# Kernel optimization log

Hardware: AMD Instinct MI355X
Metric: run time of the kernel (lower is better)

Reference implementation:

```python
import jax, jax.numpy as jnp
import numpy as np

B, H, W, C1, C2 = 4, 256, 256, 256, 128
K = 128   # cells per patch (fixed for jit; original uses torch.unique)
E = 256   # emb_dim
NC = 16   # n_classes
G = 512   # n_genes
R = 64    # n_ref
HEADS = 8


def _w(k, shape):
    return jax.random.normal(k, shape, jnp.float32) / np.float32(np.sqrt(shape[-2]))


def setup_inputs() -> dict:
    key = jax.random.key(0)
    ks = jax.random.split(key, 20)
    return {
        "hd1": jax.random.normal(ks[0], (B, C1, H, W), jnp.float32),
        "h1": jax.random.normal(ks[1], (B, C2, H, W), jnp.float32),
        "ref_orig": jax.random.uniform(ks[2], (R, G), jnp.float32),
        "embed_w": _w(ks[3], (2 * (C1 + C2), E)),
        "comp_w1": _w(ks[4], (E, E)), "comp_w2": _w(ks[5], (E, NC)),
        "hist_w1": _w(ks[6], (E, E)), "hist_w2": _w(ks[7], (E, NC)),
        "genes_w1": _w(ks[8], (G, E)), "genes_w2": _w(ks[9], (E, NC)),
        "wref_w1": _w(ks[10], (3, E, E)), "wref_w2": _w(ks[11], (3, E, R)),
        "ca_wq": _w(ks[12], (3, NC, E)), "ca_wk": _w(ks[13], (3, G, E)),
        "ca_wv": _w(ks[14], (3, G, E)), "ca_wo": _w(ks[15], (3, E, G)),
        "nuclei_mask": jax.random.randint(ks[16], (B, H, W), 0, K + 1, jnp.int32),
        "n_cells": K,
    }


def _forward(hd1, h1, ref_orig, embed_w, comp_w1, comp_w2, hist_w1, hist_w2,
             genes_w1, genes_w2, wref_w1, wref_w2, ca_wq, ca_wk, ca_wv, ca_wo,
             nuclei_mask, n_cells):
    b, c1, hgt, wid = hd1.shape
    k_cells = n_cells
    # replaces the per-cell mask-multiply-sum loop with one segment reduce
    feat = jnp.concatenate([hd1, h1], axis=1)            # [B, C1+C2, H, W]
    cf = feat.shape[1]
    feat_flat = feat.transpose(0, 2, 3, 1).reshape(b * hgt * wid, cf)
    ids = nuclei_mask.reshape(b, hgt * wid)
    seg = jnp.where(ids > 0, jnp.arange(b)[:, None] * k_cells + ids - 1,
                    b * k_cells).reshape(-1)
    nseg = b * k_cells + 1                               # last bucket = background
    sums = jax.ops.segment_sum(feat_flat, seg, num_segments=nseg)[: b * k_cells]
    area = jax.ops.segment_sum(jnp.ones((seg.shape[0],), feat.dtype), seg,
                               num_segments=nseg)[: b * k_cells]
    cell_feat = sums / jnp.maximum(area, 1.0)[:, None]   # [N, Cf]
    glob = feat.mean((2, 3))                             # [B, Cf] = fv_hd1 ++ fv_h1
    all_fv = jnp.concatenate([cell_feat, jnp.repeat(glob, k_cells, axis=0)], axis=1)
    emb = all_fv @ embed_w                               # [N, E]
    emb_patches = emb.reshape(b, k_cells, -1).mean(1)    # per-patch mean embedding
    comp = jax.nn.softmax(jax.nn.relu(emb_patches @ comp_w1) @ comp_w2, axis=-1)
    comp_tiled = jnp.repeat(comp, k_cells, axis=0)       # [N, NC]
    out_cell_type = jax.nn.relu(emb @ hist_w1) @ hist_w2

    def branch(w1, w2, wq, wk, wv, wo):
        rw = jax.nn.softmax(jax.nn.relu(emb @ w1) @ w2, axis=-1)   # [N, R]
        ref_weighted = rw @ ref_orig                               # [N, G]
        dh = wq.shape[1] // HEADS
        q = (comp_tiled @ wq).reshape(-1, HEADS, dh)
        k = (ref_weighted @ wk).reshape(-1, HEADS, dh)
        v = (ref_weighted @ wv).reshape(-1, HEADS, dh)
        attn = jax.nn.softmax(jnp.einsum("qhd,khd->hqk", q, k) / float(np.sqrt(dh)), axis=-1)
        o = jnp.einsum("hqk,khd->qhd", attn, v).reshape(-1, HEADS * dh)
        return jax.nn.relu(ref_weighted + o @ wo)

    out_exprs = jax.vmap(branch)(wref_w1, wref_w2, ca_wq, ca_wk, ca_wv, ca_wo)  # [3,N,G]
    genes_h = jax.nn.relu(out_exprs[0] @ genes_w1)
    out_cell_type_expr = genes_h @ genes_w2
    return out_cell_type, out_exprs, out_cell_type_expr, genes_h, comp, area


def reference(hd1, h1, ref_orig, embed_w, comp_w1, comp_w2, hist_w1, hist_w2,
              genes_w1, genes_w2, wref_w1, wref_w2, ca_wq, ca_wk, ca_wv, ca_wo,
              nuclei_mask, n_cells):
    out_cell_type, out_exprs, out_cell_type_expr, genes_h, comp, area = _forward(
        hd1, h1, ref_orig, embed_w, comp_w1, comp_w2, hist_w1, hist_w2,
        genes_w1, genes_w2, wref_w1, wref_w2, ca_wq, ca_wk, ca_wv, ca_wo,
        nuclei_mask, n_cells)
    return (out_cell_type, out_exprs[0], out_exprs[1], out_exprs[2],
            out_cell_type_expr, genes_h, comp, area)
```

## Files before the change

kernel.cpp:

```cpp
#include <hip/hip_runtime.h>
#include <hip/hip_bf16.h>

#define Bn 4
#define C1n 256
#define C2n 128
#define CF 384
#define HWn 65536
#define Kc 128
#define Nn 512
#define En 256
#define NCn 16
#define Gn 512
#define Rn 64
#define HEADSn 8
#define DHn 32

#define CHK 32
#define PCH2 (HWn/CHK)
#define TC2 32

#define SCALE_F 1048576.0f
#define INV_SCALE (1.0f/1048576.0f)

typedef unsigned long long ull;

__global__ __launch_bounds__(256) void area_k(const int* __restrict__ mask,
                                              int* __restrict__ apart) {
    int chunk = blockIdx.x, b = blockIdx.y;
    __shared__ int hist[4][129];
    int t = threadIdx.x, w = t >> 6;
    for (int i = t; i < 4 * 129; i += 256) ((int*)hist)[i] = 0;
    __syncthreads();
    const int* mp = mask + (size_t)b * HWn + chunk * PCH2;
    #pragma unroll
    for (int it = 0; it < PCH2 / 1024; ++it) {
        int4 v = *(const int4*)(mp + it * 1024 + t * 4);
        atomicAdd(&hist[w][v.x], 1);
        atomicAdd(&hist[w][v.y], 1);
        atomicAdd(&hist[w][v.z], 1);
        atomicAdd(&hist[w][v.w], 1);
    }
    __syncthreads();
    if (t < 128)
        apart[(chunk * Bn + b) * Kc + t] =
            hist[0][t+1] + hist[1][t+1] + hist[2][t+1] + hist[3][t+1];
}

__global__ __launch_bounds__(256) void segreduce3_k(
        const float* __restrict__ hd1, const float* __restrict__ h1,
        const int* __restrict__ mask,
        int* __restrict__ spart) {
    int chunk = blockIdx.x, cg = blockIdx.y, b = blockIdx.z;
    int c0 = cg * TC2;
    const float* base = (c0 < C1n)
        ? hd1 + ((size_t)(b * C1n + c0)) * HWn
        : h1  + ((size_t)(b * C2n + (c0 - C1n))) * HWn;
    const int* mp = mask + (size_t)b * HWn + chunk * PCH2;

    __shared__ int bins[129 * 33];

    int t = threadIdx.x;
    int cL = t >> 3, l8 = t & 7;
    for (int i = t; i < 129 * 33; i += 256) bins[i] = 0;
    __syncthreads();

    const float* rowp = base + (size_t)cL * HWn;
    for (int px0 = l8 * 4; px0 < PCH2; px0 += 64) {
        float4 v0 = *(const float4*)(rowp + px0);
        float4 v1 = *(const float4*)(rowp + px0 + 32);
        int4 i0 = *(const int4*)(mp + px0);
        int4 i1 = *(const int4*)(mp + px0 + 32);
        atomicAdd(&bins[i0.x * 33 + cL], __float2int_rn(v0.x * SCALE_F));
        atomicAdd(&bins[i0.y * 33 + cL], __float2int_rn(v0.y * SCALE_F));
        atomicAdd(&bins[i0.z * 33 + cL], __float2int_rn(v0.z * SCALE_F));
        atomicAdd(&bins[i0.w * 33 + cL], __float2int_rn(v0.w * SCALE_F));
        atomicAdd(&bins[i1.x * 33 + cL], __float2int_rn(v1.x * SCALE_F));
        atomicAdd(&bins[i1.y * 33 + cL], __float2int_rn(v1.y * SCALE_F));
        atomicAdd(&bins[i1.z * 33 + cL], __float2int_rn(v1.z * SCALE_F));
        atomicAdd(&bins[i1.w * 33 + cL], __float2int_rn(v1.w * SCALE_F));
    }
    __syncthreads();
    for (int i = t; i < 129 * TC2; i += 256) {
        int cell = i >> 5, cc = i & 31;
        spart[((size_t)(chunk * Bn + b) * 129 + cell) * CF + c0 + cc] = bins[cell * 33 + cc];
    }
}

__global__ void reduce_k(const int* __restrict__ spart, float* __restrict__ ctot) {
    int idx = blockIdx.x * 256 + threadIdx.x;
    if (idx >= Bn * 129 * CF) return;
    int b = idx / (129 * CF);
    int rem = idx - b * 129 * CF;
    long long s = 0;
    #pragma unroll 8
    for (int ch = 0; ch < CHK; ++ch)
        s += spart[((size_t)ch * Bn + b) * (129 * CF) + rem];
    ctot[idx] = (float)s * INV_SCALE;
}

__global__ void glob_k(const float* __restrict__ ctot, const int* __restrict__ apart,
                       float* __restrict__ glob,
                       float* __restrict__ areaf, float* __restrict__ area_out) {
    int idx = blockIdx.x * 256 + threadIdx.x;
    if (idx < Bn * CF) {
        int b = idx / CF, c = idx - b * CF;
        float s = 0.f;
        for (int cell = 0; cell < 129; ++cell)
            s += ctot[((size_t)(b * 129 + cell)) * CF + c];
        glob[idx] = s * (1.0f / (float)HWn);
    }
    if (idx < Nn) {
        int b = idx >> 7, cell = idx & 127;
        int s = 0;
        #pragma unroll 8
        for (int ch = 0; ch < CHK; ++ch)
            s += apart[(ch * Bn + b) * Kc + cell];
        float a = (float)s;
        areaf[idx] = a;
        area_out[idx] = a;
    }
}

__global__ __launch_bounds__(256) void gemm_emb_k(
        const float* __restrict__ ctot, const float* __restrict__ glob,
        const float* __restrict__ areaf, const float* __restrict__ Bw,
        float* __restrict__ C) {
    int row0 = blockIdx.x * 2;
    __shared__ float As[2 * 768];
    __shared__ float part[2048];
    __shared__ float rina[2];
    int t = threadIdx.x, lane = t & 63, w = t >> 6;
    if (t < 2) rina[t] = 1.f / fmaxf(areaf[row0 + t], 1.f);
    __syncthreads();
    for (int idx = t; idx < 2 * 768; idx += 256) {
        int r = idx / 768, k = idx - r * 768;
        int row = row0 + r;
        float v;
        if (k < CF) {
            int bb = row >> 7, cell = (row & 127) + 1;
            v = ctot[((size_t)(bb * 129 + cell)) * CF + k] * rina[r];
        } else {
            v = glob[(row >> 7) * CF + (k - CF)];
        }
        As[idx] = v;
    }
    __syncthreads();
    float acc[2][4] = {{0,0,0,0},{0,0,0,0}};
    const int KQ = 192;
    const float* bp = Bw + (size_t)(w * KQ) * 256 + lane * 4;
    #pragma unroll 8
    for (int k = 0; k < KQ; ++k) {
        float4 bv = *(const float4*)(bp + (size_t)k * 256);
        float a0 = As[w * KQ + k], a1 = As[768 + w * KQ + k];
        acc[0][0] = fmaf(a0, bv.x, acc[0][0]); acc[0][1] = fmaf(a0, bv.y, acc[0][1]);
        acc[0][2] = fmaf(a0, bv.z, acc[0][2]); acc[0][3] = fmaf(a0, bv.w, acc[0][3]);
        acc[1][0] = fmaf(a1, bv.x, acc[1][0]); acc[1][1] = fmaf(a1, bv.y, acc[1][1]);
        acc[1][2] = fmaf(a1, bv.z, acc[1][2]); acc[1][3] = fmaf(a1, bv.w, acc[1][3]);
    }
    *(float4*)&part[(w * 2 + 0) * 256 + lane * 4] = make_float4(acc[0][0], acc[0][1], acc[0][2], acc[0][3]);
    *(float4*)&part[(w * 2 + 1) * 256 + lane * 4] = make_float4(acc[1][0], acc[1][1], acc[1][2], acc[1][3]);
    __syncthreads();
    #pragma unroll
    for (int i2 = 0; i2 < 2; ++i2) {
        int idx = i2 * 256 + t, r = idx >> 8, c = idx & 255;
        float s = part[r*256+c] + part[(2+r)*256+c] + part[(4+r)*256+c] + part[(6+r)*256+c];
        C[(size_t)(row0 + r) * En + c] = s;
    }
}

__global__ void comp_mlp_k(const float* __restrict__ emb, const float* __restrict__ w1,
                           const float* __restrict__ w2, float* __restrict__ comp_ws,
                           float* __restrict__ comp_out) {
    int b = blockIdx.x, j = threadIdx.x;
    __shared__ float eps[En];
    __shared__ float h[En];
    __shared__ float c[NCn];
    float s0 = 0.f;
    for (int r = 0; r < Kc; r++) s0 += emb[(size_t)(b * Kc + r) * En + j];
    eps[j] = s0 * (1.f / (float)Kc);
    __syncthreads();
    float acc = 0.f;
    #pragma unroll 8
    for (int k = 0; k < En; k++) acc = fmaf(eps[k], w1[(size_t)k * En + j], acc);
    h[j] = fmaxf(acc, 0.f);
    __syncthreads();
    if (j < NCn) {
        float a2 = 0.f;
        #pragma unroll 8
        for (int k = 0; k < En; k++) a2 = fmaf(h[k], w2[(size_t)k * NCn + j], a2);
        c[j] = a2;
    }
    __syncthreads();
    if (j == 0) {
        float m = c[0];
        for (int q = 1; q < NCn; q++) m = fmaxf(m, c[q]);
        float s = 0.f;
        for (int q = 0; q < NCn; q++) { c[q] = __expf(c[q] - m); s += c[q]; }
        float inv = 1.f / s;
        for (int q = 0; q < NCn; q++) c[q] *= inv;
    }
    __syncthreads();
    if (j < NCn) {
        comp_ws[b * NCn + j] = c[j];
        comp_out[b * NCn + j] = c[j];
    }
}

__global__ __launch_bounds__(256) void fused_hist_k(
        const float* __restrict__ emb, const float* __restrict__ w1,
        const float* __restrict__ w2, float* __restrict__ out) {
    int row0 = blockIdx.x * 2;
    __shared__ float As[2 * En];
    __shared__ float part[2048];
    __shared__ float Hs[2 * En];
    int t = threadIdx.x, lane = t & 63, w = t >> 6;
    if (t < 128) *(float4*)&As[t * 4] = *(const float4*)(emb + (size_t)row0 * En + t * 4);
    __syncthreads();
    float acc[2][4] = {{0,0,0,0},{0,0,0,0}};
    const float* bp = w1 + (size_t)(w * 64) * 256 + lane * 4;
    #pragma unroll 8
    for (int k = 0; k < 64; ++k) {
        float4 bv = *(const float4*)(bp + (size_t)k * 256);
        float a0 = As[w * 64 + k], a1 = As[256 + w * 64 + k];
        acc[0][0] = fmaf(a0, bv.x, acc[0][0]); acc[0][1] = fmaf(a0, bv.y, acc[0][1]);
        acc[0][2] = fmaf(a0, bv.z, acc[0][2]); acc[0][3] = fmaf(a0, bv.w, acc[0][3]);
        acc[1][0] = fmaf(a1, bv.x, acc[1][0]); acc[1][1] = fmaf(a1, bv.y, acc[1][1]);
        acc[1][2] = fmaf(a1, bv.z, acc[1][2]); acc[1][3] = fmaf(a1, bv.w, acc[1][3]);
    }
    *(float4*)&part[(w * 2 + 0) * 256 + lane * 4] = make_float4(acc[0][0], acc[0][1], acc[0][2], acc[0][3]);
    *(float4*)&part[(w * 2 + 1) * 256 + lane * 4] = make_float4(acc[1][0], acc[1][1], acc[1][2], acc[1][3]);
    __syncthreads();
    #pragma unroll
    for (int i2 = 0; i2 < 2; ++i2) {
        int idx = i2 * 256 + t, r = idx >> 8, c = idx & 255;
        float s = part[r*256+c] + part[(2+r)*256+c] + part[(4+r)*256+c] + part[(6+r)*256+c];
        Hs[r * 256 + c] = fmaxf(s, 0.f);
    }
    __syncthreads();
    if (t < 32) {
        int r = t >> 4, j = t & 15;
        float a2 = 0.f;
        #pragma unroll 8
        for (int k = 0; k < En; k++) a2 = fmaf(Hs[r * 256 + k], w2[(size_t)k * NCn + j], a2);
        out[(size_t)(row0 + r) * NCn + j] = a2;
    }
}

__global__ __launch_bounds__(256) void fused_branch_k(
        const float* __restrict__ emb, const float* __restrict__ wref_w1,
        const float* __restrict__ wref_w2, const float* __restrict__ ref,
        float* __restrict__ refw) {
    int i = blockIdx.y, row0 = blockIdx.x * 4;
    const float* w1 = wref_w1 + (size_t)i * En * En;
    const float* w2 = wref_w2 + (size_t)i * En * Rn;
    __shared__ float As[4 * En];
    __shared__ float part[4096];
    __shared__ float Hs[4 * En];
    __shared__ float RW[4 * Rn];
    int t = threadIdx.x, lane = t & 63, w = t >> 6;
    *(float4*)&As[t * 4] = *(const float4*)(emb + (size_t)row0 * En + t * 4);
    __syncthreads();
    {
        float acc[4][4] = {{0,0,0,0},{0,0,0,0},{0,0,0,0},{0,0,0,0}};
        const float* bp = w1 + (size_t)(w * 64) * 256 + lane * 4;
        #pragma unroll 4
        for (int k = 0; k < 64; ++k) {
            float4 bv = *(const float4*)(bp + (size_t)k * 256);
            #pragma unroll
            for (int r = 0; r < 4; ++r) {
                float a = As[r * 256 + w * 64 + k];
                acc[r][0] = fmaf(a, bv.x, acc[r][0]); acc[r][1] = fmaf(a, bv.y, acc[r][1]);
                acc[r][2] = fmaf(a, bv.z, acc[r][2]); acc[r][3] = fmaf(a, bv.w, acc[r][3]);
            }
        }
        #pragma unroll
        for (int r = 0; r < 4; ++r)
            *(float4*)&part[(w * 4 + r) * 256 + lane * 4] =
                make_float4(acc[r][0], acc[r][1], acc[r][2], acc[r][3]);
    }
    __syncthreads();
    #pragma unroll
    for (int i2 = 0; i2 < 4; ++i2) {
        int idx = i2 * 256 + t, r = idx >> 8, c = idx & 255;
        float s = part[r*256+c] + part[(4+r)*256+c] + part[(8+r)*256+c] + part[(12+r)*256+c];
        Hs[r * 256 + c] = fmaxf(s, 0.f);
    }
    __syncthreads();
    {
        float a[4] = {0.f, 0.f, 0.f, 0.f};
        const float* bp = w2 + (size_t)(w * 64) * 64 + lane;
        #pragma unroll 8
        for (int k = 0; k < 64; ++k) {
            float bv = bp[(size_t)k * 64];
            #pragma unroll
            for (int r = 0; r < 4; ++r) a[r] = fmaf(Hs[r * 256 + w * 64 + k], bv, a[r]);
        }
        #pragma unroll
        for (int r = 0; r < 4; ++r) part[(w * 4 + r) * 64 + lane] = a[r];
    }
    __syncthreads();
    {
        int r = t >> 6, c = t & 63;
        RW[r * 64 + c] = part[r*64+c] + part[(4+r)*64+c] + part[(8+r)*64+c] + part[(12+r)*64+c];
    }
    __syncthreads();
    {
        float v = RW[w * 64 + lane];
        float m = v;
        #pragma unroll
        for (int o = 32; o > 0; o >>= 1) m = fmaxf(m, __shfl_xor(m, o));
        float e = __expf(v - m), s = e;
        #pragma unroll
        for (int o = 32; o > 0; o >>= 1) s += __shfl_xor(s, o);
        RW[w * 64 + lane] = e / s;
    }
    __syncthreads();
    {
        int q = t & 127, kh = t >> 7;
        float acc[4][4] = {{0,0,0,0},{0,0,0,0},{0,0,0,0},{0,0,0,0}};
        const float* bp = ref + (size_t)(kh * 32) * 512 + q * 4;
        #pragma unroll 4
        for (int k = 0; k < 32; ++k) {
            float4 bv = *(const float4*)(bp + (size_t)k * 512);
            #pragma unroll
            for (int r = 0; r < 4; ++r) {
                float a = RW[r * 64 + kh * 32 + k];
                acc[r][0] = fmaf(a, bv.x, acc[r][0]); acc[r][1] = fmaf(a, bv.y, acc[r][1]);
                acc[r][2] = fmaf(a, bv.z, acc[r][2]); acc[r][3] = fmaf(a, bv.w, acc[r][3]);
            }
        }
        #pragma unroll
        for (int r = 0; r < 4; ++r)
            *(float4*)&part[(kh * 4 + r) * 512 + q * 4] =
                make_float4(acc[r][0], acc[r][1], acc[r][2], acc[r][3]);
    }
    __syncthreads();
    float* op = refw + ((size_t)i * Nn + row0) * Gn;
    #pragma unroll
    for (int i2 = 0; i2 < 8; ++i2) {
        int idx = i2 * 256 + t, r = idx >> 9, c = idx & 511;
        op[(size_t)r * Gn + c] = part[r * 512 + c] + part[(4 + r) * 512 + c];
    }
}

__global__ __launch_bounds__(256) void fused_kv_k(
        const float* __restrict__ refw, const float* __restrict__ ca_wk,
        const float* __restrict__ ca_wv, float* __restrict__ kws,
        float* __restrict__ vws) {
    int i = blockIdx.y, row0 = blockIdx.x * 8;
    const float* wk = ca_wk + (size_t)i * Gn * En;
    const float* wv = ca_wv + (size_t)i * Gn * En;
    __shared__ float As[8 * Gn];
    __shared__ float part[8192];
    int t = threadIdx.x, lane = t & 63, w = t >> 6;
    const float* rp = refw + ((size_t)i * Nn + row0) * Gn;
    #pragma unroll
    for (int q = 0; q < 4; ++q)
        *(float4*)&As[q * 1024 + t * 4] = *(const float4*)(rp + q * 1024 + t * 4);
    __syncthreads();
    int which = w >> 1, half = w & 1;
    const float* Bp = (which ? wv : wk) + (size_t)(half * 256) * En + lane * 4;
    float acc[8][4];
    #pragma unroll
    for (int r = 0; r < 8; ++r) { acc[r][0]=0.f; acc[r][1]=0.f; acc[r][2]=0.f; acc[r][3]=0.f; }
    #pragma unroll 4
    for (int k = 0; k < 256; ++k) {
        float4 bv = *(const float4*)(Bp + (size_t)k * En);
        #pragma unroll
        for (int r = 0; r < 8; ++r) {
            float a = As[r * 512 + half * 256 + k];
            acc[r][0] = fmaf(a, bv.x, acc[r][0]); acc[r][1] = fmaf(a, bv.y, acc[r][1]);
            acc[r][2] = fmaf(a, bv.z, acc[r][2]); acc[r][3] = fmaf(a, bv.w, acc[r][3]);
        }
    }
    #pragma unroll
    for (int r = 0; r < 8; ++r)
        *(float4*)&part[(w * 8 + r) * 256 + lane * 4] =
            make_float4(acc[r][0], acc[r][1], acc[r][2], acc[r][3]);
    __syncthreads();
    #pragma unroll
    for (int i2 = 0; i2 < 8; ++i2) {
        int idx = i2 * 256 + t, r = idx >> 8, c = idx & 255;
        float sk = part[r * 256 + c] + part[(8 + r) * 256 + c];
        float sv = part[(16 + r) * 256 + c] + part[(24 + r) * 256 + c];
        kws[((size_t)i * Nn + row0 + r) * En + c] = sk;
        vws[((size_t)i * Nn + row0 + r) * En + c] = sv;
    }
}

template <int R, bool RELU>
__global__ void gemm_rows_k(const float* __restrict__ A, long long sA,
                            const float* __restrict__ Bw, long long sB,
                            float* __restrict__ C, long long sC,
                            int M, int N, int K) {
    int i = blockIdx.y;
    A += (size_t)i * sA; Bw += (size_t)i * sB; C += (size_t)i * sC;
    int row0 = blockIdx.x * R;
    extern __shared__ float As[];
    for (int idx = threadIdx.x; idx < R * K; idx += blockDim.x)
        As[idx] = A[(size_t)(row0 + idx / K) * K + (idx % K)];
    __syncthreads();
    for (int j = threadIdx.x; j < N; j += blockDim.x) {
        float acc[R];
        #pragma unroll
        for (int r = 0; r < R; r++) acc[r] = 0.f;
        const float* bp = Bw + j;
        #pragma unroll 8
        for (int k = 0; k < K; k++) {
            float bv = bp[(size_t)k * N];
            #pragma unroll
            for (int r = 0; r < R; r++) acc[r] = fmaf(As[r * K + k], bv, acc[r]);
        }
        #pragma unroll
        for (int r = 0; r < R; r++) {
            float v = acc[r];
            if (RELU) v = fmaxf(v, 0.f);
            C[(size_t)(row0 + r) * N + j] = v;
        }
    }
}

__global__ __launch_bounds__(256) void attn_k(
        const float* __restrict__ compw, const float* __restrict__ wq,
        const float* __restrict__ kmat, const float* __restrict__ vmat,
        float* __restrict__ o4) {
    int i = blockIdx.y, b = blockIdx.x & 3, h = blockIdx.x >> 2;
    const float* wqi = wq + (size_t)i * NCn * En;
    const float* km = kmat + (size_t)i * Nn * En;
    const float* vm = vmat + (size_t)i * Nn * En;
    __shared__ float q[DHn];
    __shared__ float p[Nn];
    __shared__ float red[4];
    __shared__ float pvp[8][33];
    int t = threadIdx.x;
    if (t < DHn) {
        float acc = 0.f;
        #pragma unroll
        for (int c = 0; c < NCn; c++)
            acc = fmaf(compw[b * NCn + c], wqi[(size_t)c * En + h * DHn + t], acc);
        q[t] = acc;
    }
    __syncthreads();
    const float scale = 0.17677669529663687f;
    float sv0, sv1;
    {
        const float* kr = km + (size_t)t * En + h * DHn;
        float a = 0.f;
        #pragma unroll
        for (int d = 0; d < DHn; d++) a = fmaf(q[d], kr[d], a);
        sv0 = a * scale;
        kr += (size_t)256 * En;
        a = 0.f;
        #pragma unroll
        for (int d = 0; d < DHn; d++) a = fmaf(q[d], kr[d], a);
        sv1 = a * scale;
    }
    float lm = fmaxf(sv0, sv1);
    #pragma unroll
    for (int o = 32; o > 0; o >>= 1) lm = fmaxf(lm, __shfl_xor(lm, o));
    if ((t & 63) == 0) red[t >> 6] = lm;
    __syncthreads();
    float m = fmaxf(fmaxf(red[0], red[1]), fmaxf(red[2], red[3]));
    __syncthreads();
    float e0 = __expf(sv0 - m), e1 = __expf(sv1 - m);
    p[t] = e0; p[t + 256] = e1;
    float ls = e0 + e1;
    #pragma unroll
    for (int o = 32; o > 0; o >>= 1) ls += __shfl_xor(ls, o);
    if ((t & 63) == 0) red[t >> 6] = ls;
    __syncthreads();
    float ssum = red[0] + red[1] + red[2] + red[3];
    int d = t & 31, seg = t >> 5;
    float acc = 0.f;
    const float* vp = vm + (size_t)(seg * 64) * En + h * DHn + d;
    #pragma unroll 8
    for (int j = 0; j < 64; ++j) acc = fmaf(p[seg * 64 + j], vp[(size_t)j * En], acc);
    pvp[seg][d] = acc;
    __syncthreads();
    if (t < DHn) {
        float o = 0.f;
        #pragma unroll
        for (int s8 = 0; s8 < 8; ++s8) o += pvp[s8][t];
        o4[((size_t)i * Bn + b) * En + h * DHn + t] = o / ssum;
    }
}

__global__ void add_relu_k(const float* __restrict__ refw, const float* __restrict__ ow,
                           float* __restrict__ out) {
    int i = blockIdx.y, n = blockIdx.x, b = n >> 7;
    const float4* rr = (const float4*)(refw + ((size_t)i * Nn + n) * Gn);
    const float4* oo = (const float4*)(ow + ((size_t)i * Bn + b) * Gn);
    float4* op = (float4*)(out + (size_t)i * (Nn * Gn) + (size_t)n * Gn);
    int j = threadIdx.x;
    float4 a = rr[j], o = oo[j];
    op[j] = make_float4(fmaxf(a.x + o.x, 0.f), fmaxf(a.y + o.y, 0.f),
                        fmaxf(a.z + o.z, 0.f), fmaxf(a.w + o.w, 0.f));
}

__global__ __launch_bounds__(256) void fused_genes_k(
        const float* __restrict__ e0, const float* __restrict__ gw1,
        const float* __restrict__ gw2, float* __restrict__ gh,
        float* __restrict__ octe) {
    int row0 = blockIdx.x * 2;
    __shared__ float As[2 * Gn];
    __shared__ float part[2048];
    __shared__ float Hs[2 * En];
    int t = threadIdx.x, lane = t & 63, w = t >> 6;
    *(float4*)&As[t * 4] = *(const float4*)(e0 + (size_t)row0 * Gn + t * 4);
    __syncthreads();
    {
        float acc[2][4] = {{0,0,0,0},{0,0,0,0}};
        const float* bp = gw1 + (size_t)(w * 128) * 256 + lane * 4;
        #pragma unroll 8
        for (int k = 0; k < 128; ++k) {
            float4 bv = *(const float4*)(bp + (size_t)k * 256);
            float a0 = As[w * 128 + k], a1 = As[512 + w * 128 + k];
            acc[0][0] = fmaf(a0, bv.x, acc[0][0]); acc[0][1] = fmaf(a0, bv.y, acc[0][1]);
            acc[0][2] = fmaf(a0, bv.z, acc[0][2]); acc[0][3] = fmaf(a0, bv.w, acc[0][3]);
            acc[1][0] = fmaf(a1, bv.x, acc[1][0]); acc[1][1] = fmaf(a1, bv.y, acc[1][1]);
            acc[1][2] = fmaf(a1, bv.z, acc[1][2]); acc[1][3] = fmaf(a1, bv.w, acc[1][3]);
        }
        *(float4*)&part[(w * 2 + 0) * 256 + lane * 4] = make_float4(acc[0][0], acc[0][1], acc[0][2], acc[0][3]);
        *(float4*)&part[(w * 2 + 1) * 256 + lane * 4] = make_float4(acc[1][0], acc[1][1], acc[1][2], acc[1][3]);
    }
    __syncthreads();
    #pragma unroll
    for (int i2 = 0; i2 < 2; ++i2) {
        int idx = i2 * 256 + t, r = idx >> 8, c = idx & 255;
        float s = part[r*256+c] + part[(2+r)*256+c] + part[(4+r)*256+c] + part[(6+r)*256+c];
        float v = fmaxf(s, 0.f);
        Hs[r * 256 + c] = v;
        gh[(size_t)(row0 + r) * En + c] = v;
    }
    __syncthreads();
    if (t < 32) {
        int r = t >> 4, j = t & 15;
        float a2 = 0.f;
        #pragma unroll 8
        for (int k = 0; k < En; k++) a2 = fmaf(Hs[r * 256 + k], gw2[(size_t)k * NCn + j], a2);
        octe[(size_t)(row0 + r) * NCn + j] = a2;
    }
}

extern "C" void kernel_launch(void* const* d_in, const int* in_sizes, int n_in,
                              void* d_out, int out_size, void* d_ws, size_t ws_size,
                              hipStream_t stream) {
    const float* hd1     = (const float*)d_in[0];
    const float* h1      = (const float*)d_in[1];
    const float* ref     = (const float*)d_in[2];
    const float* embed_w = (const float*)d_in[3];
    const float* comp_w1 = (const float*)d_in[4];
    const float* comp_w2 = (const float*)d_in[5];
    const float* hist_w1 = (const float*)d_in[6];
    const float* hist_w2 = (const float*)d_in[7];
    const float* genes_w1= (const float*)d_in[8];
    const float* genes_w2= (const float*)d_in[9];
    const float* wref_w1 = (const float*)d_in[10];
    const float* wref_w2 = (const float*)d_in[11];
    const float* ca_wq   = (const float*)d_in[12];
    const float* ca_wk   = (const float*)d_in[13];
    const float* ca_wv   = (const float*)d_in[14];
    const float* ca_wo   = (const float*)d_in[15];
    const int*   mask    = (const int*)d_in[16];

    float* out = (float*)d_out;
    const size_t o_ct   = 0;
    const size_t o_e0   = 8192;
    const size_t o_octe = 8192 + 3 * 262144;
    const size_t o_gh   = o_octe + 8192;
    const size_t o_comp = o_gh + 131072;
    const size_t o_area = o_comp + 64;

    int*  spart = (int*)d_ws;
    int*  apart = spart + (size_t)CHK * Bn * 129 * CF;
    float* ctot = (float*)(apart + CHK * Bn * Kc);
    float* glob = ctot + Bn * 129 * CF;
    float* areaf = glob + 1536;
    float* emb   = areaf + 512;
    float* compw = emb + 131072;
    float* refw  = compw + 64;
    float* kws   = refw + 786432;
    float* vws   = kws + 393216;
    float* o4    = vws + 393216;
    float* ow    = o4 + 3072;

    area_k<<<dim3(CHK, Bn), 256, 0, stream>>>(mask, apart);
    segreduce3_k<<<dim3(CHK, CF / TC2, Bn), 256, 0, stream>>>(hd1, h1, mask, spart);
    reduce_k<<<(Bn * 129 * CF + 255) / 256, 256, 0, stream>>>(spart, ctot);
    glob_k<<<6, 256, 0, stream>>>(ctot, apart, glob, areaf, out + o_area);
    gemm_emb_k<<<Nn / 2, 256, 0, stream>>>(ctot, glob, areaf, embed_w, emb);
    comp_mlp_k<<<Bn, 256, 0, stream>>>(emb, comp_w1, comp_w2, compw, out + o_comp);

    fused_hist_k<<<Nn / 2, 256, 0, stream>>>(emb, hist_w1, hist_w2, out + o_ct);
    fused_branch_k<<<dim3(Nn / 4, 3), 256, 0, stream>>>(emb, wref_w1, wref_w2, ref, refw);
    fused_kv_k<<<dim3(Nn / 8, 3), 256, 0, stream>>>(refw, ca_wk, ca_wv, kws, vws);
    attn_k<<<dim3(HEADSn * Bn, 3), 256, 0, stream>>>(compw, ca_wq, kws, vws, o4);
    gemm_rows_k<1, false><<<dim3(Bn, 3), 256, 256 * 4, stream>>>(
        o4, (long long)Bn * En, ca_wo, (long long)En * Gn, ow, (long long)Bn * Gn, Bn, Gn, En);
    add_relu_k<<<dim3(Nn, 3), 128, 0, stream>>>(refw, ow, out + o_e0);

    fused_genes_k<<<Nn / 2, 256, 0, stream>>>(out + o_e0, genes_w1, genes_w2,
                                              out + o_gh, out + o_octe);
}
```

Before: 646.9 us.

## Fuse tail kernels via atomics and split KV GEMM across K/V blocks

Merges glob_k into reduce_k using atomic accumulation, computes the per-batch embedding mean in gemm_emb_k with atomics, folds the output projection into attn_k, and fuses the add-relu for branch 0 into fused_genes_k. fused_kv_k now launches separate blocks for K and V so each block reduces over 128 instead of 256. A zeroing pass in area_k clears the atomic targets. The goal is fewer launches and more parallelism in the small GEMM tail, at the cost of float atomics and non-deterministic summation order.

```diff
diff --git a/kernel.cpp b/kernel.cpp
--- a/kernel.cpp
+++ b/kernel.cpp
@@ -25,10 +25,14 @@
 typedef unsigned long long ull;
 
 __global__ __launch_bounds__(256) void area_k(const int* __restrict__ mask,
-                                              int* __restrict__ apart) {
+                                              int* __restrict__ apart,
+                                              float* __restrict__ zbase) {
     int chunk = blockIdx.x, b = blockIdx.y;
     __shared__ int hist[4][129];
     int t = threadIdx.x, w = t >> 6;
+    int bid = b * CHK + chunk;
+    if (bid == 0)
+        for (int i = t; i < 8704; i += 256) zbase[i] = 0.f;
     for (int i = t; i < 4 * 129; i += 256) ((int*)hist)[i] = 0;
     __syncthreads();
     const int* mp = mask + (size_t)b * HWn + chunk * PCH2;
@@ -86,28 +90,21 @@
     }
 }
 
-__global__ void reduce_k(const int* __restrict__ spart, float* __restrict__ ctot) {
+__global__ void reduce_k(const int* __restrict__ spart, const int* __restrict__ apart,
+                         float* __restrict__ ctot, float* __restrict__ glob,
+                         float* __restrict__ areaf, float* __restrict__ area_out) {
     int idx = blockIdx.x * 256 + threadIdx.x;
-    if (idx >= Bn * 129 * CF) return;
-    int b = idx / (129 * CF);
-    int rem = idx - b * 129 * CF;
-    long long s = 0;
-    #pragma unroll 8
-    for (int ch = 0; ch < CHK; ++ch)
-        s += spart[((size_t)ch * Bn + b) * (129 * CF) + rem];
-    ctot[idx] = (float)s * INV_SCALE;
-}
-
-__global__ void glob_k(const float* __restrict__ ctot, const int* __restrict__ apart,
-                       float* __restrict__ glob,
-                       float* __restrict__ areaf, float* __restrict__ area_out) {
-    int idx = blockIdx.x * 256 + threadIdx.x;
-    if (idx < Bn * CF) {
-        int b = idx / CF, c = idx - b * CF;
-        float s = 0.f;
-        for (int cell = 0; cell < 129; ++cell)
-            s += ctot[((size_t)(b * 129 + cell)) * CF + c];
-        glob[idx] = s * (1.0f / (float)HWn);
+    if (idx < Bn * 129 * CF) {
+        int b = idx / (129 * CF);
+        int rem = idx - b * 129 * CF;
+        int cell = rem / CF, c = rem - cell * CF;
+        long long s = 0;
+        #pragma unroll 8
+        for (int ch = 0; ch < CHK; ++ch)
+            s += spart[((size_t)ch * Bn + b) * (129 * CF) + rem];
+        float val = (float)s * INV_SCALE;
+        ctot[idx] = val;
+        atomicAdd(&glob[b * CF + c], val * (1.0f / (float)HWn));
     }
     if (idx < Nn) {
         int b = idx >> 7, cell = idx & 127;
@@ -124,7 +121,7 @@
 __global__ __launch_bounds__(256) void gemm_emb_k(
         const float* __restrict__ ctot, const float* __restrict__ glob,
         const float* __restrict__ areaf, const float* __restrict__ Bw,
-        float* __restrict__ C) {
+        float* __restrict__ C, float* __restrict__ ep) {
     int row0 = blockIdx.x * 2;
     __shared__ float As[2 * 768];
     __shared__ float part[2048];
@@ -165,23 +162,19 @@
         int idx = i2 * 256 + t, r = idx >> 8, c = idx & 255;
         float s = part[r*256+c] + part[(2+r)*256+c] + part[(4+r)*256+c] + part[(6+r)*256+c];
         C[(size_t)(row0 + r) * En + c] = s;
-    }
-}
-
-__global__ void comp_mlp_k(const float* __restrict__ emb, const float* __restrict__ w1,
+        atomicAdd(&ep[((row0 + r) >> 7) * En + c], s * (1.f / (float)Kc));
+    }
+}
+
+__global__ void comp_mlp_k(const float* __restrict__ ep, const float* __restrict__ w1,
                            const float* __restrict__ w2, float* __restrict__ comp_ws,
                            float* __restrict__ comp_out) {
     int b = blockIdx.x, j = threadIdx.x;
-    __shared__ float eps[En];
     __shared__ float h[En];
     __shared__ float c[NCn];
-    float s0 = 0.f;
-    for (int r = 0; r < Kc; r++) s0 += emb[(size_t)(b * Kc + r) * En + j];
-    eps[j] = s0 * (1.f / (float)Kc);
-    __syncthreads();
     float acc = 0.f;
     #pragma unroll 8
-    for (int k = 0; k < En; k++) acc = fmaf(eps[k], w1[(size_t)k * En + j], acc);
+    for (int k = 0; k < En; k++) acc = fmaf(ep[b * En + k], w1[(size_t)k * En + j], acc);
     h[j] = fmaxf(acc, 0.f);
     __syncthreads();
     if (j < NCn) {
@@ -347,9 +340,9 @@
         const float* __restrict__ refw, const float* __restrict__ ca_wk,
         const float* __restrict__ ca_wv, float* __restrict__ kws,
         float* __restrict__ vws) {
-    int i = blockIdx.y, row0 = blockIdx.x * 8;
-    const float* wk = ca_wk + (size_t)i * Gn * En;
-    const float* wv = ca_wv + (size_t)i * Gn * En;
+    int i = blockIdx.z, which = blockIdx.y, row0 = blockIdx.x * 8;
+    const float* W = (which ? ca_wv : ca_wk) + (size_t)i * Gn * En;
+    float* outp = (which ? vws : kws) + ((size_t)i * Nn + row0) * En;
     __shared__ float As[8 * Gn];
     __shared__ float part[8192];
     int t = threadIdx.x, lane = t & 63, w = t >> 6;
@@ -358,17 +351,16 @@
     for (int q = 0; q < 4; ++q)
         *(float4*)&As[q * 1024 + t * 4] = *(const float4*)(rp + q * 1024 + t * 4);
     __syncthreads();
-    int which = w >> 1, half = w & 1;
-    const float* Bp = (which ? wv : wk) + (size_t)(half * 256) * En + lane * 4;
+    const float* Bp = W + (size_t)(w * 128) * En + lane * 4;
     float acc[8][4];
     #pragma unroll
     for (int r = 0; r < 8; ++r) { acc[r][0]=0.f; acc[r][1]=0.f; acc[r][2]=0.f; acc[r][3]=0.f; }
     #pragma unroll 4
-    for (int k = 0; k < 256; ++k) {
+    for (int k = 0; k < 128; ++k) {
         float4 bv = *(const float4*)(Bp + (size_t)k * En);
         #pragma unroll
         for (int r = 0; r < 8; ++r) {
-            float a = As[r * 512 + half * 256 + k];
+            float a = As[r * 512 + w * 128 + k];
             acc[r][0] = fmaf(a, bv.x, acc[r][0]); acc[r][1] = fmaf(a, bv.y, acc[r][1]);
             acc[r][2] = fmaf(a, bv.z, acc[r][2]); acc[r][3] = fmaf(a, bv.w, acc[r][3]);
         }
@@ -381,49 +373,16 @@
     #pragma unroll
     for (int i2 = 0; i2 < 8; ++i2) {
         int idx = i2 * 256 + t, r = idx >> 8, c = idx & 255;
-        float sk = part[r * 256 + c] + part[(8 + r) * 256 + c];
-        float sv = part[(16 + r) * 256 + c] + part[(24 + r) * 256 + c];
-        kws[((size_t)i * Nn + row0 + r) * En + c] = sk;
-        vws[((size_t)i * Nn + row0 + r) * En + c] = sv;
-    }
-}
-
-template <int R, bool RELU>
-__global__ void gemm_rows_k(const float* __restrict__ A, long long sA,
-                            const float* __restrict__ Bw, long long sB,
-                            float* __restrict__ C, long long sC,
-                            int M, int N, int K) {
-    int i = blockIdx.y;
-    A += (size_t)i * sA; Bw += (size_t)i * sB; C += (size_t)i * sC;
-    int row0 = blockIdx.x * R;
-    extern __shared__ float As[];
-    for (int idx = threadIdx.x; idx < R * K; idx += blockDim.x)
-        As[idx] = A[(size_t)(row0 + idx / K) * K + (idx % K)];
-    __syncthreads();
-    for (int j = threadIdx.x; j < N; j += blockDim.x) {
-        float acc[R];
-        #pragma unroll
-        for (int r = 0; r < R; r++) acc[r] = 0.f;
-        const float* bp = Bw + j;
-        #pragma unroll 8
-        for (int k = 0; k < K; k++) {
-            float bv = bp[(size_t)k * N];
-            #pragma unroll
-            for (int r = 0; r < R; r++) acc[r] = fmaf(As[r * K + k], bv, acc[r]);
-        }
-        #pragma unroll
-        for (int r = 0; r < R; r++) {
-            float v = acc[r];
-            if (RELU) v = fmaxf(v, 0.f);
-            C[(size_t)(row0 + r) * N + j] = v;
-        }
+        float s = part[r * 256 + c] + part[(8 + r) * 256 + c]
+                + part[(16 + r) * 256 + c] + part[(24 + r) * 256 + c];
+        outp[(size_t)r * En + c] = s;
     }
 }
 
 __global__ __launch_bounds__(256) void attn_k(
         const float* __restrict__ compw, const float* __restrict__ wq,
         const float* __restrict__ kmat, const float* __restrict__ vmat,
-        float* __restrict__ o4) {
+        const float* __restrict__ ca_wo, float* __restrict__ ow) {
     int i = blockIdx.y, b = blockIdx.x & 3, h = blockIdx.x >> 2;
     const float* wqi = wq + (size_t)i * NCn * En;
     const float* km = kmat + (size_t)i * Nn * En;
@@ -432,6 +391,7 @@
     __shared__ float p[Nn];
     __shared__ float red[4];
     __shared__ float pvp[8][33];
+    __shared__ float of[DHn];
     int t = threadIdx.x;
     if (t < DHn) {
         float acc = 0.f;
@@ -481,13 +441,27 @@
         float o = 0.f;
         #pragma unroll
         for (int s8 = 0; s8 < 8; ++s8) o += pvp[s8][t];
-        o4[((size_t)i * Bn + b) * En + h * DHn + t] = o / ssum;
+        of[t] = o / ssum;
+    }
+    __syncthreads();
+    {
+        const float* wop = ca_wo + ((size_t)i * En + h * DHn) * Gn;
+        float a0 = 0.f, a1 = 0.f;
+        #pragma unroll
+        for (int dd = 0; dd < DHn; ++dd) {
+            float ov = of[dd];
+            a0 = fmaf(ov, wop[(size_t)dd * Gn + t], a0);
+            a1 = fmaf(ov, wop[(size_t)dd * Gn + t + 256], a1);
+        }
+        float* owp = ow + ((size_t)i * Bn + b) * Gn;
+        atomicAdd(&owp[t], a0);
+        atomicAdd(&owp[t + 256], a1);
     }
 }
 
 __global__ void add_relu_k(const float* __restrict__ refw, const float* __restrict__ ow,
                            float* __restrict__ out) {
-    int i = blockIdx.y, n = blockIdx.x, b = n >> 7;
+    int i = blockIdx.y + 1, n = blockIdx.x, b = n >> 7;
     const float4* rr = (const float4*)(refw + ((size_t)i * Nn + n) * Gn);
     const float4* oo = (const float4*)(ow + ((size_t)i * Bn + b) * Gn);
     float4* op = (float4*)(out + (size_t)i * (Nn * Gn) + (size_t)n * Gn);
@@ -498,15 +472,25 @@
 }
 
 __global__ __launch_bounds__(256) void fused_genes_k(
-        const float* __restrict__ e0, const float* __restrict__ gw1,
-        const float* __restrict__ gw2, float* __restrict__ gh,
+        const float* __restrict__ refw, const float* __restrict__ ow,
+        const float* __restrict__ gw1, const float* __restrict__ gw2,
+        float* __restrict__ e0, float* __restrict__ gh,
         float* __restrict__ octe) {
     int row0 = blockIdx.x * 2;
     __shared__ float As[2 * Gn];
     __shared__ float part[2048];
     __shared__ float Hs[2 * En];
     int t = threadIdx.x, lane = t & 63, w = t >> 6;
-    *(float4*)&As[t * 4] = *(const float4*)(e0 + (size_t)row0 * Gn + t * 4);
+    {
+        int idx4 = t * 4, r = idx4 >> 9, c = idx4 & 511;
+        int row = row0 + r, b = row >> 7;
+        float4 a = *(const float4*)(refw + (size_t)row * Gn + c);
+        float4 o = *(const float4*)(ow + (size_t)b * Gn + c);
+        float4 v = make_float4(fmaxf(a.x + o.x, 0.f), fmaxf(a.y + o.y, 0.f),
+                               fmaxf(a.z + o.z, 0.f), fmaxf(a.w + o.w, 0.f));
+        *(float4*)&As[idx4] = v;
+        *(float4*)(e0 + (size_t)row * Gn + c) = v;
+    }
     __syncthreads();
     {
         float acc[2][4] = {{0,0,0,0},{0,0,0,0}};
@@ -575,30 +559,27 @@
     int*  apart = spart + (size_t)CHK * Bn * 129 * CF;
     float* ctot = (float*)(apart + CHK * Bn * Kc);
     float* glob = ctot + Bn * 129 * CF;
-    float* areaf = glob + 1536;
+    float* ep   = glob + 1536;
+    float* ow   = ep + 1024;
+    float* areaf = ow + 6144;
     float* emb   = areaf + 512;
     float* compw = emb + 131072;
     float* refw  = compw + 64;
     float* kws   = refw + 786432;
     float* vws   = kws + 393216;
-    float* o4    = vws + 393216;
-    float* ow    = o4 + 3072;
-
-    area_k<<<dim3(CHK, Bn), 256, 0, stream>>>(mask, apart);
+
+    area_k<<<dim3(CHK, Bn), 256, 0, stream>>>(mask, apart, glob);
     segreduce3_k<<<dim3(CHK, CF / TC2, Bn), 256, 0, stream>>>(hd1, h1, mask, spart);
-    reduce_k<<<(Bn * 129 * CF + 255) / 256, 256, 0, stream>>>(spart, ctot);
-    glob_k<<<6, 256, 0, stream>>>(ctot, apart, glob, areaf, out + o_area);
-    gemm_emb_k<<<Nn / 2, 256, 0, stream>>>(ctot, glob, areaf, embed_w, emb);
-    comp_mlp_k<<<Bn, 256, 0, stream>>>(emb, comp_w1, comp_w2, compw, out + o_comp);
-
+    reduce_k<<<(Bn * 129 * CF + 255) / 256, 256, 0, stream>>>(
+        spart, apart, ctot, glob, areaf, out + o_area);
+    gemm_emb_k<<<Nn / 2, 256, 0, stream>>>(ctot, glob, areaf, embed_w, emb, ep);
+    comp_mlp_k<<<Bn, 256, 0, stream>>>(ep, comp_w1, comp_w2, compw, out + o_comp);
+
+    fused_branch_k<<<dim3(Nn / 4, 3), 256, 0, stream>>>(emb, wref_w1, wref_w2, ref, refw);
+    fused_kv_k<<<dim3(Nn / 8, 2, 3), 256, 0, stream>>>(refw, ca_wk, ca_wv, kws, vws);
+    attn_k<<<dim3(HEADSn * Bn, 3), 256, 0, stream>>>(compw, ca_wq, kws, vws, ca_wo, ow);
+    add_relu_k<<<dim3(Nn, 2), 128, 0, stream>>>(refw, ow, out + o_e0);
+    fused_genes_k<<<Nn / 2, 256, 0, stream>>>(refw, ow, genes_w1, genes_w2,
+                                              out + o_e0, out + o_gh, out + o_octe);
     fused_hist_k<<<Nn / 2, 256, 0, stream>>>(emb, hist_w1, hist_w2, out + o_ct);
-    fused_branch_k<<<dim3(Nn / 4, 3), 256, 0, stream>>>(emb, wref_w1, wref_w2, ref, refw);
-    fused_kv_k<<<dim3(Nn / 8, 3), 256, 0, stream>>>(refw, ca_wk, ca_wv, kws, vws);
-    attn_k<<<dim3(HEADSn * Bn, 3), 256, 0, stream>>>(compw, ca_wq, kws, vws, o4);
-    gemm_rows_k<1, false><<<dim3(Bn, 3), 256, 256 * 4, stream>>>(
-        o4, (long long)Bn * En, ca_wo, (long long)En * Gn, ow, (long long)Bn * Gn, Bn, Gn, En);
-    add_relu_k<<<dim3(Nn, 3), 128, 0, stream>>>(refw, ow, out + o_e0);
-
-    fused_genes_k<<<Nn / 2, 256, 0, stream>>>(out + o_e0, genes_w1, genes_w2,
-                                              out + o_gh, out + o_octe);
-}
+}
```

Measured after the change: 579.3 us. 10.5% less time.
